# Optimization experiments

Hardware: AMD Instinct MI355X
Metric: run time of the kernel (lower is better)

## Reference

```python
import jax, jax.numpy as jnp
import numpy as np

GROUPS = 16
EPS = 1e-6


def group_norm(x, gamma, beta):
    b, c, h, w = x.shape
    xg = x.reshape(b, GROUPS, c // GROUPS, h, w)
    mean = xg.mean(axis=(2, 3, 4), keepdims=True)
    var = xg.var(axis=(2, 3, 4), keepdims=True)
    xn = ((xg - mean) * jax.lax.rsqrt(var + EPS)).reshape(b, c, h, w)
    return xn * gamma[None, :, None, None] + beta[None, :, None, None]


def conv1x1(x, w, b):
    # x: [B,C,H,W], w: [O,C], b: [O]
    return jnp.einsum('bchw,oc->bohw', x, w) + b[None, :, None, None]


def setup_inputs() -> dict:
    key = jax.random.key(0)
    ks = jax.random.split(key, 10)
    C = 256
    x = jax.random.normal(ks[0], (4, C, 64, 64), dtype=jnp.float32)
    s = 1.0 / np.sqrt(C)
    return {
        'x': x,
        'gamma': jnp.ones((C,), jnp.float32),
        'beta': jnp.zeros((C,), jnp.float32),
        'wq': jax.random.normal(ks[1], (C, C), jnp.float32) * s,
        'bq': jnp.zeros((C,), jnp.float32),
        'wk': jax.random.normal(ks[2], (C, C), jnp.float32) * s,
        'bk': jnp.zeros((C,), jnp.float32),
        'wv': jax.random.normal(ks[3], (C, C), jnp.float32) * s,
        'bv': jnp.zeros((C,), jnp.float32),
        'wp': jax.random.normal(ks[4], (C, C), jnp.float32) * s,
        'bp': jnp.zeros((C,), jnp.float32),
    }


def reference(x, gamma, beta, wq, bq, wk, bk, wv, bv, wp, bp):
    b, c, h, w = x.shape
    hn = group_norm(x, gamma, beta)
    q = conv1x1(hn, wq, bq).reshape(b, c, h * w)   # [B,C,N]
    k = conv1x1(hn, wk, bk).reshape(b, c, h * w)
    v = conv1x1(hn, wv, bv).reshape(b, c, h * w)
    # scores[b,i,j] = sum_c q[b,c,i] * k[b,c,j], scaled by c^-0.5
    scores = jnp.einsum('bci,bcj->bij', q, k) * (c ** -0.5)
    attn = jax.nn.softmax(scores, axis=2)           # [B,N,N]
    # h_out[b,c,i] = sum_j v[b,c,j] * attn[b,i,j]
    h_out = jnp.einsum('bcj,bij->bci', v, attn).reshape(b, c, h, w)
    return x + conv1x1(h_out, wp, bp)
```

## Files before the change

### kernel.cpp

```cpp
#include <hip/hip_runtime.h>

#define B_ 4
#define C_ 256
#define N_ 4096
#define K2_ 0.09016844f
#define THR_ 64.0f

typedef __attribute__((ext_vector_type(8))) short short8;
typedef __attribute__((ext_vector_type(4))) float f32x4;
typedef __attribute__((ext_vector_type(16))) float f32x16;
typedef __attribute__((ext_vector_type(4))) unsigned int uint4v;

static __device__ __forceinline__ short f2bf(float f) {
  union { float f; unsigned u; } v; v.f = f;
  unsigned r = v.u + 0x7FFFu + ((v.u >> 16) & 1u);
  return (short)(r >> 16);
}
static __device__ __forceinline__ float bf2f(short s) {
  union { unsigned u; float f; } v; v.u = ((unsigned)(unsigned short)s) << 16;
  return v.f;
}
static __device__ __forceinline__ f32x4 mfma16(short8 a, short8 b, f32x4 c) {
  return __builtin_amdgcn_mfma_f32_16x16x32_bf16(a, b, c, 0, 0, 0);
}
static __device__ __forceinline__ f32x16 mfma32(short8 a, short8 b, f32x16 c) {
  return __builtin_amdgcn_mfma_f32_32x32x16_bf16(a, b, c, 0, 0, 0);
}
static __device__ __forceinline__ unsigned cvtpk(float lo, float hi) {
  unsigned r;
  asm("v_cvt_pk_bf16_f32 %0, %1, %2" : "=v"(r) : "v"(lo), "v"(hi));
  return r;
}
static __device__ __forceinline__ void plswap(unsigned& a, unsigned& b) {
  asm volatile("v_permlane32_swap_b32 %0, %1" : "+v"(a), "+v"(b));
}
static __device__ __forceinline__ void gload16(const void* g, void* l) {
  __builtin_amdgcn_global_load_lds(
      (const __attribute__((address_space(1))) unsigned int*)g,
      (__attribute__((address_space(3))) unsigned int*)l, 16, 0, 0);
}

__global__ __launch_bounds__(256) void prep(const float* __restrict__ x,
                                            const float* __restrict__ wq,
                                            const float* __restrict__ wk,
                                            const float* __restrict__ wv,
                                            const float* __restrict__ wp,
                                            float2* __restrict__ part,
                                            short* __restrict__ wout) {
  if (blockIdx.x >= 256) {
    int idx = (blockIdx.x - 256) * 256 + threadIdx.x;
    int which = idx >> 16, e = idx & 65535;
    const float* src = which == 0 ? wq : which == 1 ? wk : which == 2 ? wv : wp;
    wout[(which << 16) + e] = f2bf(src[e]);
    return;
  }
  int bg = blockIdx.x >> 2, ch = blockIdx.x & 3;
  const float* xp = x + (long)bg * 65536 + ch * 16384;
  int t = threadIdx.x, lane = t & 63, w = t >> 6;
  float s = 0.f, ss = 0.f;
  for (int e = t * 4; e < 16384; e += 1024) {
    f32x4 v = *(const f32x4*)(xp + e);
    s += (v[0] + v[1]) + (v[2] + v[3]);
    ss += (v[0] * v[0] + v[1] * v[1]) + (v[2] * v[2] + v[3] * v[3]);
  }
  for (int off = 1; off < 64; off <<= 1) {
    s += __shfl_xor(s, off);
    ss += __shfl_xor(ss, off);
  }
  __shared__ float rs[4], rq[4];
  if (lane == 0) { rs[w] = s; rq[w] = ss; }
  __syncthreads();
  if (t == 0)
    part[blockIdx.x] = make_float2((rs[0] + rs[1]) + (rs[2] + rs[3]),
                                   (rq[0] + rq[1]) + (rq[2] + rq[3]));
}

__global__ __launch_bounds__(256) void gn_norm(const float* __restrict__ x,
                                               const float* __restrict__ gamma,
                                               const float* __restrict__ beta,
                                               const float2* __restrict__ part,
                                               short* __restrict__ hn) {
  int ic = blockIdx.x, g = blockIdx.y, b = blockIdx.z;
  int bg = b * 16 + g;
  float2 q0 = part[bg * 4], q1 = part[bg * 4 + 1], q2 = part[bg * 4 + 2], q3 = part[bg * 4 + 3];
  float s = (q0.x + q1.x) + (q2.x + q3.x);
  float ss = (q0.y + q1.y) + (q2.y + q3.y);
  float mean = s * (1.f / 65536.f);
  float rstd = rsqrtf(ss * (1.f / 65536.f) - mean * mean + 1e-6f);
  int t = threadIdx.x;
  int i = ic * 256 + t;
  __shared__ short Ls[16][256];
#pragma unroll
  for (int cl = 0; cl < 16; cl++) {
    int c = g * 16 + cl;
    float v = x[((long)(b * 256 + c)) * N_ + i];
    Ls[cl][t] = f2bf((v - mean) * rstd * gamma[c] + beta[c]);
  }
  __syncthreads();
  short8 v0, v1;
#pragma unroll
  for (int q = 0; q < 8; q++) { v0[q] = Ls[q][t]; v1[q] = Ls[8 + q][t]; }
  short* dst = hn + ((long)b * N_ + ic * 256 + t) * C_ + g * 16;
  *(short8*)dst = v0;
  *(short8*)(dst + 8) = v1;
}

__global__ __launch_bounds__(256) void gemm_qkv(const short* __restrict__ hn,
                                                const short* __restrict__ wqkv,
                                                const float* __restrict__ bq,
                                                const float* __restrict__ bk,
                                                const float* __restrict__ bv,
                                                short* __restrict__ qT,
                                                short* __restrict__ kT,
                                                short* __restrict__ vbM) {
  __shared__ __align__(16) short As[3][128 * 32];
  __shared__ __align__(16) short Bs[3][128 * 32];
  const int bz = blockIdx.z;
  const int n0 = blockIdx.x * 128;
  const int m0 = blockIdx.y * 128;
  const int t = threadIdx.x, lane = t & 63, w = t >> 6;
  const int wm = (w >> 1) * 64, wn = (w & 1) * 64;
  const short* Ab = hn + (long)bz * N_ * C_;
  f32x4 acc[4][4];
#pragma unroll
  for (int m = 0; m < 4; m++)
#pragma unroll
    for (int n = 0; n < 4; n++) acc[m][n] = (f32x4)0.f;
  const int g16 = (lane >> 4) * 16;

  auto stage = [&](int kt8, int buf) {
    int kt = kt8 * 32;
#pragma unroll
    for (int s = 0; s < 2; s++) {
      int q = w * 2 + s;
      int flat = q * 1024 + lane * 16;
      int row = flat >> 6, c = flat & 63;
      int cs = c ^ ((row & 3) << 4);
      gload16((const char*)Ab + ((long)(m0 + row) * 256 + kt) * 2 + cs, (char*)As[buf] + flat);
      gload16((const char*)wqkv + ((long)(n0 + row) * 256 + kt) * 2 + cs, (char*)Bs[buf] + flat);
    }
  };

  stage(0, 0);
  for (int kt8 = 0; kt8 < 8; kt8++) {
    const int cur = kt8 % 3;
    if (kt8 < 7) {
      stage(kt8 + 1, (kt8 + 1) % 3);
      asm volatile("s_waitcnt vmcnt(4)" ::: "memory");
    } else {
      asm volatile("s_waitcnt vmcnt(0)" ::: "memory");
    }
    __builtin_amdgcn_s_barrier();
    __builtin_amdgcn_sched_barrier(0);
    short8 af[4], bf[4];
#pragma unroll
    for (int m = 0; m < 4; m++) {
      int row = wm + m * 16 + (lane & 15);
      af[m] = *(const short8*)(&As[cur][0] + row * 32 + ((g16 ^ ((row & 3) << 4)) >> 1));
    }
#pragma unroll
    for (int n = 0; n < 4; n++) {
      int row = wn + n * 16 + (lane & 15);
      bf[n] = *(const short8*)(&Bs[cur][0] + row * 32 + ((g16 ^ ((row & 3) << 4)) >> 1));
    }
    __builtin_amdgcn_s_setprio(1);
#pragma unroll
    for (int m = 0; m < 4; m++)
#pragma unroll
      for (int n = 0; n < 4; n++) acc[m][n] = mfma16(af[m], bf[n], acc[m][n]);
    __builtin_amdgcn_s_setprio(0);
  }

  int seg = n0 >> 8;
  const float* bias = seg == 0 ? bq : seg == 1 ? bk : bv;
#pragma unroll
  for (int m = 0; m < 4; m++)
#pragma unroll
    for (int n = 0; n < 4; n++)
#pragma unroll
      for (int r = 0; r < 4; r++) {
        int row = m0 + wm + m * 16 + ((lane >> 4) << 2) + r;
        int colg = n0 + wn + n * 16 + (lane & 15);
        int coll = colg & 255;
        float vv = acc[m][n][r] + bias[coll];
        if (seg == 2) vbM[(long)bz * N_ * C_ + (long)coll * N_ + row] = f2bf(vv);
        else (seg == 0 ? qT : kT)[(long)bz * N_ * C_ + (long)row * 256 + coll] = f2bf(vv);
      }
}

__global__ __launch_bounds__(256) void gemm_proj(const short* __restrict__ wp,
                                                 const short* __restrict__ hT,
                                                 const float* __restrict__ bp,
                                                 const float* __restrict__ x,
                                                 float* __restrict__ out) {
  __shared__ __align__(16) short As[3][128 * 32];
  __shared__ __align__(16) short Bs[3][128 * 32];
  const int bz = blockIdx.z;
  const int n0 = blockIdx.x * 128;
  const int m0 = blockIdx.y * 128;
  const int t = threadIdx.x, lane = t & 63, w = t >> 6;
  const int wm = (w >> 1) * 64, wn = (w & 1) * 64;
  const short* Bb = hT + (long)bz * N_ * C_;
  f32x4 acc[4][4];
#pragma unroll
  for (int m = 0; m < 4; m++)
#pragma unroll
    for (int n = 0; n < 4; n++) acc[m][n] = (f32x4)0.f;
  const int g16 = (lane >> 4) * 16;

  auto stage = [&](int kt8, int buf) {
    int kt = kt8 * 32;
#pragma unroll
    for (int s = 0; s < 2; s++) {
      int q = w * 2 + s;
      int flat = q * 1024 + lane * 16;
      int row = flat >> 6, c = flat & 63;
      int cs = c ^ ((row & 3) << 4);
      gload16((const char*)wp + ((long)(m0 + row) * 256 + kt) * 2 + cs, (char*)As[buf] + flat);
      gload16((const char*)Bb + ((long)(n0 + row) * 256 + kt) * 2 + cs, (char*)Bs[buf] + flat);
    }
  };

  stage(0, 0);
  for (int kt8 = 0; kt8 < 8; kt8++) {
    const int cur = kt8 % 3;
    if (kt8 < 7) {
      stage(kt8 + 1, (kt8 + 1) % 3);
      asm volatile("s_waitcnt vmcnt(4)" ::: "memory");
    } else {
      asm volatile("s_waitcnt vmcnt(0)" ::: "memory");
    }
    __builtin_amdgcn_s_barrier();
    __builtin_amdgcn_sched_barrier(0);
    short8 af[4], bf[4];
#pragma unroll
    for (int m = 0; m < 4; m++) {
      int row = wm + m * 16 + (lane & 15);
      af[m] = *(const short8*)(&As[cur][0] + row * 32 + ((g16 ^ ((row & 3) << 4)) >> 1));
    }
#pragma unroll
    for (int n = 0; n < 4; n++) {
      int row = wn + n * 16 + (lane & 15);
      bf[n] = *(const short8*)(&Bs[cur][0] + row * 32 + ((g16 ^ ((row & 3) << 4)) >> 1));
    }
    __builtin_amdgcn_s_setprio(1);
#pragma unroll
    for (int m = 0; m < 4; m++)
#pragma unroll
      for (int n = 0; n < 4; n++) acc[m][n] = mfma16(af[m], bf[n], acc[m][n]);
    __builtin_amdgcn_s_setprio(0);
  }

#pragma unroll
  for (int m = 0; m < 4; m++)
#pragma unroll
    for (int n = 0; n < 4; n++)
#pragma unroll
      for (int r = 0; r < 4; r++) {
        int row = m0 + wm + m * 16 + ((lane >> 4) << 2) + r;
        int col = n0 + wn + n * 16 + (lane & 15);
        long idx = (long)bz * N_ * C_ + (long)row * N_ + col;
        out[idx] = acc[m][n][r] + bp[row] + x[idx];
      }
}

__global__ __launch_bounds__(256, 2) void attn_kernel(
    const short* __restrict__ qT, const short* __restrict__ kT,
    const short* __restrict__ vM, short* __restrict__ P0, short* __restrict__ P1,
    short* __restrict__ P2, short* __restrict__ P3, float2* __restrict__ ml, int S) {
  __shared__ __align__(16) char kv[3 * 16384];
  __shared__ float cbr[4][32];

  const int nwg = 128 * S;
  const int id = blockIdx.x;
  const int nid = (id & 7) * (nwg >> 3) + (id >> 3);
  const int itile = nid & 31;
  const int bjs = nid >> 5;
  const int js = bjs % S;
  const int b = bjs / S;

  const int t = threadIdx.x, lane = t & 63, w = t >> 6;
  const int hi = lane >> 5, li = lane & 31;
  const int hi16 = hi * 16;
  const int lsw = li << 4;
  const long bNC = (long)b * N_ * C_;
  const short* qb = qT + bNC;
  const char* kb = (const char*)(kT + bNC);
  const char* vbp = (const char*)(vM + bNC);
  const int i0 = itile * 128 + w * 32;
  const int jbase = js * (N_ / S);
  const int NIT = (N_ / S) / 32;

  short8 qf[16];
  {
    const short* qp = qb + (long)(i0 + li) * C_ + hi * 8;
#pragma unroll
    for (int s = 0; s < 16; s++) qf[s] = *(const short8*)(qp + s * 16);
  }

  f32x16 acco[8];
#pragma unroll
  for (int cb = 0; cb < 8; cb++) acco[cb] = (f32x16)0.f;
  float m_run = -3e38f, l_run = 0.f;

  auto stage = [&](int it, int vb) {
    const int j0 = jbase + it * 32;
    char* Kd = kv;
    char* Vd = kv + 16384 + vb * 16384;
#pragma unroll
    for (int p = 0; p < 4; p++) {
      int flat = p * 4096 + t * 16;
      int rk = flat >> 9;
      int cO = (flat & 511) ^ ((rk & 31) << 4);
      gload16(kb + (long)(j0 + rk) * 512 + cO, Kd + flat);
    }
#pragma unroll
    for (int p = 0; p < 4; p++) {
      int flat = p * 4096 + t * 16;
      int rv = flat >> 9;
      int cO = (flat & 511) ^ ((rv & 31) << 4);
      int c = rv + ((cO >> 6) << 5);
      int off = cO & 63;
      gload16(vbp + (long)c * 8192 + (long)j0 * 2 + off, Vd + flat);
    }
  };

  auto smpack = [&](f32x16& accs, short8& paA, short8& paB) {
    float pm[8];
#pragma unroll
    for (int r = 0; r < 8; r++) pm[r] = fmaxf(accs[2 * r], accs[2 * r + 1]);
#pragma unroll
    for (int r = 0; r < 4; r++) pm[r] = fmaxf(pm[2 * r], pm[2 * r + 1]);
    float pmax = fmaxf(fmaxf(pm[0], pm[1]), fmaxf(pm[2], pm[3]));
    pmax = fmaxf(pmax, __shfl_xor(pmax, 32));
    if (__any(pmax > m_run + THR_)) {
      float mnew = fmaxf(m_run, pmax);
      float corr = exp2f((m_run - mnew) * K2_);
      m_run = mnew;
      l_run *= corr;
      if (lane < 32) cbr[w][li] = corr;
      asm volatile("s_waitcnt lgkmcnt(0)" ::: "memory");
      f32x4 c4[4];
#pragma unroll
      for (int g = 0; g < 4; g++) c4[g] = *(const f32x4*)&cbr[w][g * 8 + hi * 4];
#pragma unroll
      for (int cb = 0; cb < 8; cb++)
#pragma unroll
        for (int r = 0; r < 16; r++) acco[cb][r] *= c4[r >> 2][r & 3];
    }
    const float mk = m_run * K2_;
    float p[16];
#pragma unroll
    for (int r = 0; r < 16; r++) {
      p[r] = exp2f(fmaf(accs[r], K2_, -mk));
      l_run += p[r];
    }
    unsigned a0 = cvtpk(p[0], p[1]), b0 = cvtpk(p[4], p[5]);
    unsigned a1 = cvtpk(p[2], p[3]), b1 = cvtpk(p[6], p[7]);
    plswap(a0, b0); plswap(a1, b1);
    uint4v u0 = {a0, a1, b0, b1};
    paA = __builtin_bit_cast(short8, u0);
    unsigned a2 = cvtpk(p[8], p[9]), b2 = cvtpk(p[12], p[13]);
    unsigned a3 = cvtpk(p[10], p[11]), b3 = cvtpk(p[14], p[15]);
    plswap(a2, b2); plswap(a3, b3);
    uint4v u1 = {a2, a3, b2, b3};
    paB = __builtin_bit_cast(short8, u1);
  };

  const char* Kr = kv + li * 512;

  stage(0, 0);
  __syncthreads();
  f32x16 accs = (f32x16)0.f;
  __builtin_amdgcn_s_setprio(1);
#pragma unroll
  for (int s = 0; s < 16; s++) {
    short8 kf = *(const short8*)(Kr + ((s * 32 + hi16) ^ lsw));
    accs = mfma32(kf, qf[s], accs);
  }
  __builtin_amdgcn_s_setprio(0);

  short8 pa0, pa1;
  for (int it = 1; it < NIT; it++) {
    __syncthreads();
    stage(it, it & 1);
    smpack(accs, pa0, pa1);
    asm volatile("s_waitcnt vmcnt(4)" ::: "memory");
    __builtin_amdgcn_s_barrier();
    const char* Vr = kv + 16384 + ((it - 1) & 1) * 16384 + li * 512;
    f32x16 a2 = (f32x16)0.f;
    __builtin_amdgcn_s_setprio(1);
#pragma unroll
    for (int u = 0; u < 8; u++) {
      short8 kfa = *(const short8*)(Kr + (((2 * u) * 32 + hi16) ^ lsw));
      a2 = mfma32(kfa, qf[2 * u], a2);
      short8 vf0 = *(const short8*)(Vr + ((u * 64 + hi16) ^ lsw));
      acco[u] = mfma32(pa0, vf0, acco[u]);
      short8 kfb = *(const short8*)(Kr + (((2 * u + 1) * 32 + hi16) ^ lsw));
      a2 = mfma32(kfb, qf[2 * u + 1], a2);
      short8 vf1 = *(const short8*)(Vr + ((u * 64 + 32 + hi16) ^ lsw));
      acco[u] = mfma32(pa1, vf1, acco[u]);
    }
    __builtin_amdgcn_s_setprio(0);
    accs = a2;
  }

  smpack(accs, pa0, pa1);
  asm volatile("s_waitcnt vmcnt(0)" ::: "memory");
  __builtin_amdgcn_s_barrier();
  {
    const char* Vr = kv + 16384 + ((NIT - 1) & 1) * 16384 + li * 512;
    __builtin_amdgcn_s_setprio(1);
#pragma unroll
    for (int cb = 0; cb < 8; cb++) {
      short8 vf0 = *(const short8*)(Vr + ((cb * 64 + hi16) ^ lsw));
      acco[cb] = mfma32(pa0, vf0, acco[cb]);
      short8 vf1 = *(const short8*)(Vr + ((cb * 64 + 32 + hi16) ^ lsw));
      acco[cb] = mfma32(pa1, vf1, acco[cb]);
    }
    __builtin_amdgcn_s_setprio(0);
  }

  l_run += __shfl_xor(l_run, 32);
  float inv = 1.f / l_run;
  if (lane < 32) cbr[w][li] = inv;
  asm volatile("s_waitcnt lgkmcnt(0)" ::: "memory");
  f32x4 i4[4];
#pragma unroll
  for (int g = 0; g < 4; g++) i4[g] = *(const f32x4*)&cbr[w][g * 8 + hi * 4];

  short* Op = (js == 0) ? P0 : (js == 1) ? P1 : (js == 2) ? P2 : P3;
  short* ob = Op + bNC;
#pragma unroll
  for (int cb = 0; cb < 8; cb++)
#pragma unroll
    for (int r = 0; r < 16; r++) {
      int i = i0 + (r & 3) + 8 * (r >> 2) + 4 * hi;
      ob[(long)i * C_ + cb * 32 + li] = f2bf(acco[cb][r] * i4[r >> 2][r & 3]);
    }
  if (lane < 32)
    ml[(long)js * (B_ * N_) + b * N_ + i0 + li] = make_float2(m_run * K2_, l_run);
}

__global__ __launch_bounds__(256) void combine(const short* __restrict__ p0,
                                               const short* __restrict__ p1,
                                               const short* __restrict__ p2,
                                               const short* __restrict__ p3,
                                               const float2* __restrict__ ml, int S,
                                               short* __restrict__ hT) {
  int idx = blockIdx.x * 256 + threadIdx.x;
  int row = idx >> 5, c0 = (idx & 31) * 8;
  float2 m0 = ml[row], m1 = ml[16384 + row];
  float mmax = fmaxf(m0.x, m1.x);
  float2 m2 = m0, m3 = m0;
  if (S == 4) {
    m2 = ml[2 * 16384 + row];
    m3 = ml[3 * 16384 + row];
    mmax = fmaxf(mmax, fmaxf(m2.x, m3.x));
  }
  float w0 = m0.y * exp2f(m0.x - mmax);
  float w1 = m1.y * exp2f(m1.x - mmax);
  float w2 = 0.f, w3 = 0.f;
  if (S == 4) { w2 = m2.y * exp2f(m2.x - mmax); w3 = m3.y * exp2f(m3.x - mmax); }
  float inv = 1.f / ((w0 + w1) + (w2 + w3));
  w0 *= inv; w1 *= inv; w2 *= inv; w3 *= inv;
  long off = (long)row * 256 + c0;
  short8 u0 = *(const short8*)(p0 + off);
  short8 u1 = *(const short8*)(p1 + off);
  short8 o;
  if (S == 4) {
    short8 u2 = *(const short8*)(p2 + off);
    short8 u3 = *(const short8*)(p3 + off);
#pragma unroll
    for (int j = 0; j < 8; j++)
      o[j] = f2bf((w0 * bf2f(u0[j]) + w1 * bf2f(u1[j])) +
                  (w2 * bf2f(u2[j]) + w3 * bf2f(u3[j])));
  } else {
#pragma unroll
    for (int j = 0; j < 8; j++) o[j] = f2bf(w0 * bf2f(u0[j]) + w1 * bf2f(u1[j]));
  }
  *(short8*)(hT + off) = o;
}

extern "C" void kernel_launch(void* const* d_in, const int* in_sizes, int n_in,
                              void* d_out, int out_size, void* d_ws, size_t ws_size,
                              hipStream_t stream) {
  const float* x = (const float*)d_in[0];
  const float* gamma = (const float*)d_in[1];
  const float* beta = (const float*)d_in[2];
  const float* wq = (const float*)d_in[3];
  const float* bq = (const float*)d_in[4];
  const float* wk = (const float*)d_in[5];
  const float* bk = (const float*)d_in[6];
  const float* wv = (const float*)d_in[7];
  const float* bv = (const float*)d_in[8];
  const float* wp = (const float*)d_in[9];
  const float* bp = (const float*)d_in[10];

  char* ws = (char*)d_ws;
  short* hn = (short*)ws;
  short* qT = (short*)(ws + (size_t)8388608);
  short* kT = (short*)(ws + (size_t)16777216);
  short* vb = (short*)(ws + (size_t)25165824);
  short* wqkv = (short*)(ws + (size_t)33554432);
  short* wpb = wqkv + 3 * 65536;
  float2* part = (float2*)(ws + (size_t)34078720);
  float2* ml = (float2*)(ws + (size_t)34080768);
  short* P1 = (short*)d_out;
  short* P2 = (short*)d_out + 4194304;
  short* P3 = (short*)(ws + (size_t)34605056);
  const int S = (ws_size >= (size_t)43000000) ? 4 : 2;
  if (S == 2) { P2 = hn; P3 = hn; }

  prep<<<1280, 256, 0, stream>>>(x, wq, wk, wv, wp, part, wqkv);
  gn_norm<<<dim3(16, 16, 4), 256, 0, stream>>>(x, gamma, beta, part, hn);

  gemm_qkv<<<dim3(6, 32, 4), 256, 0, stream>>>(hn, wqkv, bq, bk, bv, qT, kT, vb);

  attn_kernel<<<dim3(128 * S), 256, 0, stream>>>(qT, kT, vb, hn , P1, P2, P3, ml, S);
  combine<<<2048, 256, 0, stream>>>(hn, P1, P2, P3, ml, S, hn );

  gemm_proj<<<dim3(32, 2, 4), 256, 0, stream>>>(wpb, hn, bp, x, (float*)d_out);
}
```

Measured before the change: 161.3 us.

## Fuse split-KV combine into output projection GEMM B-operand staging

Adds a projection GEMM that loads the four split-attention partial outputs, merges them with per-row softmax max/sum weights, and writes the merged bf16 tile straight into shared memory. The separate combine kernel and its round trip of the merged activation through global memory go away. When the workspace is large enough, partial buffers move from the output buffer into the workspace. In exchange, each GEMM block reads four partial tiles, and the merge arithmetic is repeated by the two blocks that share a column tile.

```diff
diff --git a/kernel.cpp b/kernel.cpp
--- a/kernel.cpp
+++ b/kernel.cpp
@@ -264,6 +264,130 @@
       }
 }
 
+__global__ __launch_bounds__(256) void gemm_proj_f(
+    const short* __restrict__ wp, const short* __restrict__ p0,
+    const short* __restrict__ p1, const short* __restrict__ p2,
+    const short* __restrict__ p3, const float2* __restrict__ ml,
+    const float* __restrict__ bp, const float* __restrict__ x,
+    float* __restrict__ out) {
+  __shared__ __align__(16) short As[2][128 * 32];
+  __shared__ __align__(16) short Bs[2][128 * 32];
+  const int bz = blockIdx.z;
+  const int n0 = blockIdx.x * 128;
+  const int m0 = blockIdx.y * 128;
+  const int t = threadIdx.x, lane = t & 63, w = t >> 6;
+  const int wm = (w >> 1) * 64, wn = (w & 1) * 64;
+  f32x4 acc[4][4];
+#pragma unroll
+  for (int m = 0; m < 4; m++)
+#pragma unroll
+    for (int n = 0; n < 4; n++) acc[m][n] = (f32x4)0.f;
+  const int g16 = (lane >> 4) * 16;
+
+  int flat_[2], soff_[2];
+  long rowg_[2];
+  float wt_[2][4];
+#pragma unroll
+  for (int s = 0; s < 2; s++) {
+    int flat = (w * 2 + s) * 1024 + lane * 16;
+    int rowl = flat >> 6, c = flat & 63;
+    int cs = c ^ ((rowl & 3) << 4);
+    flat_[s] = flat;
+    soff_[s] = cs >> 1;
+    long rowg = (long)bz * 4096 + n0 + rowl;
+    rowg_[s] = rowg;
+    float2 a0 = ml[rowg], a1 = ml[16384 + rowg];
+    float2 a2 = ml[2 * 16384 + rowg], a3 = ml[3 * 16384 + rowg];
+    float mm = fmaxf(fmaxf(a0.x, a1.x), fmaxf(a2.x, a3.x));
+    float w0 = a0.y * exp2f(a0.x - mm);
+    float w1 = a1.y * exp2f(a1.x - mm);
+    float w2 = a2.y * exp2f(a2.x - mm);
+    float w3 = a3.y * exp2f(a3.x - mm);
+    float inv = 1.f / ((w0 + w1) + (w2 + w3));
+    wt_[s][0] = w0 * inv; wt_[s][1] = w1 * inv;
+    wt_[s][2] = w2 * inv; wt_[s][3] = w3 * inv;
+  }
+
+  auto stage_A = [&](int kt8, int buf) {
+    int kt = kt8 * 32;
+#pragma unroll
+    for (int s = 0; s < 2; s++) {
+      int flat = (w * 2 + s) * 1024 + lane * 16;
+      int row = flat >> 6, c = flat & 63;
+      int cs = c ^ ((row & 3) << 4);
+      gload16((const char*)wp + ((long)(m0 + row) * 256 + kt) * 2 + cs, (char*)As[buf] + flat);
+    }
+  };
+
+  short8 u_[2][4];
+  auto ld_B = [&](int kt8) {
+    int kt = kt8 * 32;
+#pragma unroll
+    for (int s = 0; s < 2; s++) {
+      long base = rowg_[s] * 256 + kt + soff_[s];
+      u_[s][0] = *(const short8*)(p0 + base);
+      u_[s][1] = *(const short8*)(p1 + base);
+      u_[s][2] = *(const short8*)(p2 + base);
+      u_[s][3] = *(const short8*)(p3 + base);
+    }
+  };
+  auto wr_B = [&](int buf) {
+#pragma unroll
+    for (int s = 0; s < 2; s++) {
+      short8 o;
+#pragma unroll
+      for (int j = 0; j < 8; j++)
+        o[j] = f2bf((wt_[s][0] * bf2f(u_[s][0][j]) + wt_[s][1] * bf2f(u_[s][1][j])) +
+                    (wt_[s][2] * bf2f(u_[s][2][j]) + wt_[s][3] * bf2f(u_[s][3][j])));
+      *(short8*)((char*)Bs[buf] + flat_[s]) = o;
+    }
+  };
+
+  ld_B(0);
+  stage_A(0, 0);
+  wr_B(0);
+  __syncthreads();
+
+  for (int kt8 = 0; kt8 < 8; kt8++) {
+    const int cur = kt8 & 1;
+    if (kt8 < 7) {
+      ld_B(kt8 + 1);
+      stage_A(kt8 + 1, cur ^ 1);
+    }
+    short8 af[4], bf[4];
+#pragma unroll
+    for (int m = 0; m < 4; m++) {
+      int row = wm + m * 16 + (lane & 15);
+      af[m] = *(const short8*)(&As[cur][0] + row * 32 + ((g16 ^ ((row & 3) << 4)) >> 1));
+    }
+#pragma unroll
+    for (int n = 0; n < 4; n++) {
+      int row = wn + n * 16 + (lane & 15);
+      bf[n] = *(const short8*)(&Bs[cur][0] + row * 32 + ((g16 ^ ((row & 3) << 4)) >> 1));
+    }
+    __builtin_amdgcn_s_setprio(1);
+#pragma unroll
+    for (int m = 0; m < 4; m++)
+#pragma unroll
+      for (int n = 0; n < 4; n++) acc[m][n] = mfma16(af[m], bf[n], acc[m][n]);
+    __builtin_amdgcn_s_setprio(0);
+    if (kt8 < 7) wr_B(cur ^ 1);
+    __syncthreads();
+  }
+
+#pragma unroll
+  for (int m = 0; m < 4; m++)
+#pragma unroll
+    for (int n = 0; n < 4; n++)
+#pragma unroll
+      for (int r = 0; r < 4; r++) {
+        int row = m0 + wm + m * 16 + ((lane >> 4) << 2) + r;
+        int col = n0 + wn + n * 16 + (lane & 15);
+        long idx = (long)bz * N_ * C_ + (long)row * N_ + col;
+        out[idx] = acc[m][n][r] + bp[row] + x[idx];
+      }
+}
+
 __global__ __launch_bounds__(256, 2) void attn_kernel(
     const short* __restrict__ qT, const short* __restrict__ kT,
     const short* __restrict__ vM, short* __restrict__ P0, short* __restrict__ P1,
@@ -506,9 +630,10 @@
   short* wpb = wqkv + 3 * 65536;
   float2* part = (float2*)(ws + (size_t)34078720);
   float2* ml = (float2*)(ws + (size_t)34080768);
-  short* P1 = (short*)d_out;
-  short* P2 = (short*)d_out + 4194304;
   short* P3 = (short*)(ws + (size_t)34605056);
+  const bool FUSE = (ws_size >= (size_t)59770880);
+  short* P1 = FUSE ? (short*)(ws + (size_t)42993664) : (short*)d_out;
+  short* P2 = FUSE ? (short*)(ws + (size_t)51382272) : ((short*)d_out + 4194304);
   const int S = (ws_size >= (size_t)43000000) ? 4 : 2;
   if (S == 2) { P2 = hn; P3 = hn; }
 
@@ -518,7 +643,12 @@
   gemm_qkv<<<dim3(6, 32, 4), 256, 0, stream>>>(hn, wqkv, bq, bk, bv, qT, kT, vb);
 
   attn_kernel<<<dim3(128 * S), 256, 0, stream>>>(qT, kT, vb, hn , P1, P2, P3, ml, S);
-  combine<<<2048, 256, 0, stream>>>(hn, P1, P2, P3, ml, S, hn );
-
-  gemm_proj<<<dim3(32, 2, 4), 256, 0, stream>>>(wpb, hn, bp, x, (float*)d_out);
-}
+
+  if (FUSE && S == 4) {
+    gemm_proj_f<<<dim3(32, 2, 4), 256, 0, stream>>>(wpb, hn, P1, P2, P3, ml, bp, x,
+                                                    (float*)d_out);
+  } else {
+    combine<<<2048, 256, 0, stream>>>(hn, P1, P2, P3, ml, S, hn );
+    gemm_proj<<<dim3(32, 2, 4), 256, 0, stream>>>(wpb, hn, bp, x, (float*)d_out);
+  }
+}
```

Result: no change. 161.6 us (+0.2%).
